# Optimization experiments

Hardware: AMD Instinct MI355X
Metric: run time of the kernel (lower is better)

The kernel has to match this reference:

```python
import jax, jax.numpy as jnp
import numpy as np

N_USERS = 100000
N_ITEMS = 50000
D = 64
IMG_D = 1024
TXT_D = 384
N_EDGES = 2000000
GNN_LAYERS = 2
CAT_RATE = 0.55
NORM_SCALE = 1.0


def setup_inputs() -> dict:
    key = jax.random.key(0)
    ks = jax.random.split(key, 12)
    return {
        "image_feats": jax.random.normal(ks[0], (N_ITEMS, IMG_D), jnp.float32),
        "text_feats": jax.random.normal(ks[1], (N_ITEMS, TXT_D), jnp.float32),
        "user_emb": jax.random.normal(ks[2], (N_USERS, D), jnp.float32) * 0.1,
        "item_emb": jax.random.normal(ks[3], (N_ITEMS, D), jnp.float32) * 0.1,
        "W_img": jax.random.normal(ks[4], (IMG_D, D), jnp.float32) / np.sqrt(IMG_D),
        "b_img": jnp.zeros((D,), jnp.float32),
        "W_txt": jax.random.normal(ks[5], (TXT_D, D), jnp.float32) / np.sqrt(TXT_D),
        "b_txt": jnp.zeros((D,), jnp.float32),
        "val_ui": jax.random.uniform(ks[6], (N_EDGES,), jnp.float32) * 0.05,
        "val_iu": jax.random.uniform(ks[7], (N_EDGES,), jnp.float32) * 0.05,
        "edge_u": jax.random.randint(ks[8], (N_EDGES,), 0, N_USERS, jnp.int32),
        "edge_i": jax.random.randint(ks[9], (N_EDGES,), 0, N_ITEMS, jnp.int32),
    }


def _l2norm(x, eps=1e-12):
    # F.normalize(x, p=2, dim=1)
    n = jnp.maximum(jnp.linalg.norm(x, axis=1, keepdims=True), eps)
    return x / n


def reference(image_feats, text_feats, user_emb, item_emb,
              W_img, b_img, W_txt, b_txt, val_ui, val_iu, edge_u, edge_i):
    def spmm_ui(X):  # ui_graph @ X : [n_items, d] -> [n_users, d]
        return jax.ops.segment_sum(val_ui[:, None] * X[edge_i], edge_u,
                                   num_segments=N_USERS)

    def spmm_iu(X):  # iu_graph @ X : [n_users, d] -> [n_items, d]
        return jax.ops.segment_sum(val_iu[:, None] * X[edge_u], edge_i,
                                   num_segments=N_ITEMS)

    # prompt_module is None -> prompt_user/prompt_item are zeros, so the
    # feat_prompt terms (normalize of zeros) vanish. Dropout in eval = identity.
    image_feat = image_feats @ W_img + b_img  # [n_items, D]
    text_feat = text_feats @ W_txt + b_txt    # [n_items, D]

    # The original loop recomputes identical values every iteration (image_feat
    # is never updated), so one pass gives the same result.
    image_user = spmm_ui(image_feat)
    image_item = spmm_iu(image_user)
    text_user = spmm_ui(text_feat)
    text_item = spmm_iu(text_user)

    # soft_token_rate * normalize(zeros) == 0 -> id embeddings unchanged
    combined = jnp.concatenate([user_emb, item_emb], axis=0)
    # NormLayer mode 'PN' (PairNorm): center, then scale by mean row norm
    c = combined - combined.mean(axis=0, keepdims=True)
    rownorm_mean = jnp.sqrt(jnp.mean(jnp.sum(c * c, axis=1)) + 1e-6)
    normed = NORM_SCALE * c / rownorm_mean
    u_g, i_g = normed[:N_USERS], normed[N_USERS:]

    u_acc, i_acc = u_g, i_g
    for _ in range(GNN_LAYERS):  # is_softmax=False branch
        u_g = spmm_ui(i_g)
        i_g = spmm_iu(u_g)
        u_acc = u_acc + u_g
        i_acc = i_acc + i_g
    user_embeddings = u_acc / (GNN_LAYERS + 1)
    item_embeddings = i_acc / (GNN_LAYERS + 1)

    u_out = (user_embeddings + CAT_RATE * _l2norm(image_user)
             + CAT_RATE * _l2norm(text_user))
    i_out = (item_embeddings + CAT_RATE * _l2norm(image_item)
             + CAT_RATE * _l2norm(text_item))
    return (u_out, i_out, image_item, text_item, image_user, text_user)
```

## Files before the change

kernel.cpp:

```cpp
#include <hip/hip_runtime.h>
#include <cstdint>
#include <cstddef>

#define N_USERS 100000
#define N_ITEMS 50000
#define DIM     64
#define IMG_D   1024
#define TXT_D   384
#define N_EDGES 2000000
#define N_COMB  (N_USERS + N_ITEMS)

#define OFF_UOUT 0
#define OFF_IOUT (N_USERS * DIM)
#define OFF_IIT  (OFF_IOUT + N_ITEMS * DIM)
#define OFF_TIT  (OFF_IIT + N_ITEMS * DIM)
#define OFF_IUS  (OFF_TIT + N_ITEMS * DIM)
#define OFF_TUS  (OFF_IUS + N_USERS * DIM)

typedef __attribute__((ext_vector_type(8))) short short8;
typedef __attribute__((ext_vector_type(4))) float float4v;
typedef __attribute__((ext_vector_type(4))) unsigned int uint4v;

__device__ __forceinline__ float wave_sum64(float v) {
#pragma unroll
  for (int off = 32; off; off >>= 1) v += __shfl_xor(v, off, 64);
  return v;
}

__device__ __forceinline__ unsigned int pack_bf16(float x, float y) {
  const unsigned int xu = __float_as_uint(x) + 0x8000u;
  const unsigned int yu = __float_as_uint(y) + 0x8000u;
  return (xu >> 16) | (yu & 0xffff0000u);
}

__device__ __forceinline__ float4v fma4(float w, const float4v x, float4v a) {
#pragma unroll
  for (int j = 0; j < 4; ++j) a[j] = fmaf(w, x[j], a[j]);
  return a;
}

__global__ __launch_bounds__(256) void hist_kernel(const int* __restrict__ eu,
                                                   const int* __restrict__ ei,
                                                   int* __restrict__ cu, int* __restrict__ ci,
                                                   int* __restrict__ pe_u, int* __restrict__ pe_i) {
  const int i = blockIdx.x * 256 + threadIdx.x;
  if (i < N_EDGES) {
    pe_u[i] = atomicAdd(&cu[eu[i]], 1);
    pe_i[i] = atomicAdd(&ci[ei[i]], 1);
  }
}

__global__ __launch_bounds__(1024) void scan2_kernel(const int* __restrict__ cnt_u,
                                                     int* __restrict__ rs_u,
                                                     const int* __restrict__ cnt_i,
                                                     int* __restrict__ rs_i) {
  const int* counts;
  int *rs, n;
  if (blockIdx.x == 0) { counts = cnt_u; rs = rs_u; n = N_USERS; }
  else                 { counts = cnt_i; rs = rs_i; n = N_ITEMS; }
  __shared__ int part[1024];
  const int t = threadIdx.x;
  const int chunk = (n + 1023) >> 10;
  const int b = t * chunk;
  const int e = min(b + chunk, n);
  int s = 0;
  for (int j = b; j < e; ++j) s += counts[j];
  part[t] = s;
  __syncthreads();
  for (int off = 1; off < 1024; off <<= 1) {
    const int add = (t >= off) ? part[t - off] : 0;
    __syncthreads();
    part[t] += add;
    __syncthreads();
  }
  int run = (t == 0) ? 0 : part[t - 1];
  for (int j = b; j < e; ++j) {
    rs[j] = run;
    run += counts[j];
  }
  if (t == 1023) rs[n] = part[1023];
}

__global__ __launch_bounds__(256) void fill_kernel(
    const int* __restrict__ eu, const int* __restrict__ ei,
    const float* __restrict__ vui, const float* __restrict__ viu,
    const int* __restrict__ pe_u, const int* __restrict__ pe_i,
    const int* __restrict__ rs_u, const int* __restrict__ rs_i,
    int* __restrict__ col_u, float* __restrict__ w_u,
    int* __restrict__ col_i, float* __restrict__ w_i) {
  const int i = blockIdx.x * 256 + threadIdx.x;
  if (i < N_EDGES) {
    const int u = eu[i], it = ei[i];
    const int p = rs_u[u] + pe_u[i];
    const int q = rs_i[it] + pe_i[i];
    col_u[p] = it;
    w_u[p] = vui[i];
    col_i[q] = u;
    w_i[q] = viu[i];
  }
}

__global__ __launch_bounds__(256) void wswizzle_kernel(const float* __restrict__ Wimg,
                                                       const float* __restrict__ Wtxt,
                                                       unsigned short* __restrict__ WBimg,
                                                       unsigned short* __restrict__ WBtxt) {
  int t = blockIdx.x * 256 + threadIdx.x;
  const float* W;
  unsigned short* WB;
  if (t < 8192) { W = Wimg; WB = WBimg; }
  else if (t < 8192 + 3072) { t -= 8192; W = Wtxt; WB = WBtxt; }
  else return;
  const int frag = t >> 6;
  const int lane = t & 63;
  const int K0idx = frag >> 2;
  const int n0idx = frag & 3;
  const int k0 = K0idx * 32 + ((lane >> 4) << 3);
  const int c = n0idx * 16 + (lane & 15);
  unsigned short us[8];
#pragma unroll
  for (int j = 0; j < 8; ++j) {
    const unsigned int b = __float_as_uint(W[(size_t)(k0 + j) * 64 + c]) + 0x8000u;
    us[j] = (unsigned short)(b >> 16);
  }
  uint4v o;
  o.x = (unsigned int)us[0] | ((unsigned int)us[1] << 16);
  o.y = (unsigned int)us[2] | ((unsigned int)us[3] << 16);
  o.z = (unsigned int)us[4] | ((unsigned int)us[5] << 16);
  o.w = (unsigned int)us[6] | ((unsigned int)us[7] << 16);
  *reinterpret_cast<uint4v*>(WB + (size_t)t * 8) = o;
}

__global__ __launch_bounds__(256) void mfma_gemm_kernel(
    const float* __restrict__ Ximg, const unsigned short* __restrict__ WBimg,
    const float* __restrict__ bimg,
    const float* __restrict__ Xtxt, const unsigned short* __restrict__ WBtxt,
    const float* __restrict__ btxt,
    float* __restrict__ feat128) {
  const int TILES_IMG = N_ITEMS / 16;
  const int wv = threadIdx.x >> 6;
  const int lane = threadIdx.x & 63;
  int tile = blockIdx.x * 4 + wv;
  if (tile >= 2 * TILES_IMG) return;

  const float* X;
  const unsigned short* WB;
  const float* bias;
  int K, nK0, c0;
  if (tile < TILES_IMG) { X = Ximg; WB = WBimg; bias = bimg; K = IMG_D; nK0 = IMG_D / 32; c0 = 0; }
  else { tile -= TILES_IMG; X = Xtxt; WB = WBtxt; bias = btxt; K = TXT_D; nK0 = TXT_D / 32; c0 = 64; }

  const int row0 = tile * 16;
  const int m = lane & 15;
  const int koff = (lane >> 4) << 3;
  const float* __restrict__ xp = X + (size_t)(row0 + m) * K + koff;
  const short8* __restrict__ wb8 = reinterpret_cast<const short8*>(WB);

  float4v acc[4];
#pragma unroll
  for (int n0 = 0; n0 < 4; ++n0) acc[n0] = (float4v){0.f, 0.f, 0.f, 0.f};

  for (int K0 = 0; K0 < nK0; ++K0) {
    const float4 xa = *reinterpret_cast<const float4*>(xp + K0 * 32);
    const float4 xb = *reinterpret_cast<const float4*>(xp + K0 * 32 + 4);
    uint4v au;
    au.x = pack_bf16(xa.x, xa.y);
    au.y = pack_bf16(xa.z, xa.w);
    au.z = pack_bf16(xb.x, xb.y);
    au.w = pack_bf16(xb.z, xb.w);
    const short8 af = __builtin_bit_cast(short8, au);
#pragma unroll
    for (int n0 = 0; n0 < 4; ++n0) {
      const short8 bf = wb8[(size_t)(K0 * 4 + n0) * 64 + lane];
      acc[n0] = __builtin_amdgcn_mfma_f32_16x16x32_bf16(af, bf, acc[n0], 0, 0, 0);
    }
  }

  const int crow = (lane >> 4) << 2;
  const int ccol = lane & 15;
#pragma unroll
  for (int n0 = 0; n0 < 4; ++n0) {
    const float bv = bias[n0 * 16 + ccol];
#pragma unroll
    for (int r = 0; r < 4; ++r) {
      feat128[(size_t)(row0 + crow + r) * 128 + c0 + n0 * 16 + ccol] = acc[n0][r] + bv;
    }
  }
}

__global__ __launch_bounds__(256) void stats_kernel(const float* __restrict__ ue,
                                                    const float* __restrict__ ie,
                                                    float* __restrict__ stats) {
  const int t = threadIdx.x;
  const int lane = t & 63;
  float cs = 0.f, ss = 0.f;
  const size_t total = (size_t)N_COMB * DIM;
  const size_t ubound = (size_t)N_USERS * DIM;
  const size_t stride = (size_t)gridDim.x * blockDim.x;
  for (size_t i = (size_t)blockIdx.x * blockDim.x + t; i < total; i += stride) {
    const float v = (i < ubound) ? ue[i] : ie[i - ubound];
    cs += v;
    ss += v * v;
  }
  ss = wave_sum64(ss);
  __shared__ float lcol[4][64];
  __shared__ float lss[4];
  const int wv = t >> 6;
  lcol[wv][lane] = cs;
  if (lane == 0) lss[wv] = ss;
  __syncthreads();
  if (wv == 0) {
    const float c = lcol[0][lane] + lcol[1][lane] + lcol[2][lane] + lcol[3][lane];
    atomicAdd(&stats[lane], c);
    if (lane == 0) atomicAdd(&stats[64], lss[0] + lss[1] + lss[2] + lss[3]);
  }
}

__global__ void finalize_kernel(float* __restrict__ stats) {
  const int d = threadIdx.x;
  const float ssum = stats[64];
  const float m = stats[d] / (float)N_COMB;
  const float m2sum = wave_sum64(m * m);
  const float tot = ssum - (float)N_COMB * m2sum;
  const float rnm = sqrtf(tot / (float)N_COMB + 1e-6f);
  stats[d] = m;
  if (d == 0) stats[64] = 1.f / rnm;
}

__global__ __launch_bounds__(256) void normalize_kernel(
    const float* __restrict__ ue, const float* __restrict__ ie, const float* __restrict__ stats,
    float* __restrict__ uacc, float* __restrict__ iacc, float* __restrict__ i0) {
  const int lane = threadIdx.x & 63;
  const float m = stats[lane];
  const float inv = stats[64];
  const size_t total = (size_t)N_COMB * DIM;
  const size_t ubound = (size_t)N_USERS * DIM;
  const size_t stride = (size_t)gridDim.x * blockDim.x;
  for (size_t i = (size_t)blockIdx.x * blockDim.x + threadIdx.x; i < total; i += stride) {
    if (i < ubound) {
      uacc[i] = (ue[i] - m) * inv;
    } else {
      const size_t j = i - ubound;
      const float v = (ie[j] - m) * inv;
      iacc[j] = v;
      i0[j] = v;
    }
  }
}

__global__ __launch_bounds__(256) void spmm_triple_kernel(
    const int* __restrict__ rs, const int* __restrict__ col, const float* __restrict__ w,
    const float* __restrict__ X1, int s1, const float* __restrict__ X2, int s2,
    const float* __restrict__ X3, int s3,
    float* __restrict__ O1, float* __restrict__ O2, float* __restrict__ O3,
    float* __restrict__ acc, int nrows) {
  const int lane = threadIdx.x & 63;
  const int wv = __builtin_amdgcn_readfirstlane(threadIdx.x >> 6);
  const int r = blockIdx.x * 4 + wv;
  if (r >= nrows) return;
  const int q = lane >> 4;
  const int l = lane & 15;
  const int s = rs[r], e = rs[r + 1];
  float4v a1 = {0.f, 0.f, 0.f, 0.f};
  float4v a2 = {0.f, 0.f, 0.f, 0.f};
  float4v a3 = {0.f, 0.f, 0.f, 0.f};
  int k = s + q;
  for (; k + 4 < e; k += 8) {
    const int c0 = col[k];
    const int c1 = col[k + 4];
    const float w0 = w[k];
    const float w1 = w[k + 4];
    const float4v x10 = *reinterpret_cast<const float4v*>(X1 + (size_t)c0 * s1 + l * 4);
    const float4v x20 = *reinterpret_cast<const float4v*>(X2 + (size_t)c0 * s2 + l * 4);
    const float4v x30 = *reinterpret_cast<const float4v*>(X3 + (size_t)c0 * s3 + l * 4);
    const float4v x11 = *reinterpret_cast<const float4v*>(X1 + (size_t)c1 * s1 + l * 4);
    const float4v x21 = *reinterpret_cast<const float4v*>(X2 + (size_t)c1 * s2 + l * 4);
    const float4v x31 = *reinterpret_cast<const float4v*>(X3 + (size_t)c1 * s3 + l * 4);
    a1 = fma4(w0, x10, a1);
    a2 = fma4(w0, x20, a2);
    a3 = fma4(w0, x30, a3);
    a1 = fma4(w1, x11, a1);
    a2 = fma4(w1, x21, a2);
    a3 = fma4(w1, x31, a3);
  }
  if (k < e) {
    const float w0 = w[k];
    const int c0 = col[k];
    a1 = fma4(w0, *reinterpret_cast<const float4v*>(X1 + (size_t)c0 * s1 + l * 4), a1);
    a2 = fma4(w0, *reinterpret_cast<const float4v*>(X2 + (size_t)c0 * s2 + l * 4), a2);
    a3 = fma4(w0, *reinterpret_cast<const float4v*>(X3 + (size_t)c0 * s3 + l * 4), a3);
  }
#pragma unroll
  for (int j = 0; j < 4; ++j) {
    a1[j] += __shfl_xor(a1[j], 16, 64);
    a1[j] += __shfl_xor(a1[j], 32, 64);
    a2[j] += __shfl_xor(a2[j], 16, 64);
    a2[j] += __shfl_xor(a2[j], 32, 64);
    a3[j] += __shfl_xor(a3[j], 16, 64);
    a3[j] += __shfl_xor(a3[j], 32, 64);
  }
  if (q == 0) {
    const size_t o = (size_t)r * 64 + l * 4;
    *reinterpret_cast<float4v*>(O1 + o) = a1;
    *reinterpret_cast<float4v*>(O2 + o) = a2;
    *reinterpret_cast<float4v*>(O3 + o) = a3;
    float4v av = *reinterpret_cast<const float4v*>(acc + o);
#pragma unroll
    for (int j = 0; j < 4; ++j) av[j] += a3[j];
    *reinterpret_cast<float4v*>(acc + o) = av;
  }
}

__global__ __launch_bounds__(256) void spmm_final_kernel(
    const int* __restrict__ rs, const int* __restrict__ col, const float* __restrict__ w,
    const float* __restrict__ X, float* __restrict__ O,
    const float* __restrict__ P, const float* __restrict__ Q,
    float* __restrict__ accio, int nrows) {
  const int lane = threadIdx.x & 63;
  const int wv = __builtin_amdgcn_readfirstlane(threadIdx.x >> 6);
  const int r = blockIdx.x * 4 + wv;
  if (r >= nrows) return;
  const int q = lane >> 4;
  const int l = lane & 15;
  const int s = rs[r], e = rs[r + 1];
  float4v a = {0.f, 0.f, 0.f, 0.f};
  int k = s + q;
  for (; k + 4 < e; k += 8) {
    const int c0 = col[k];
    const int c1 = col[k + 4];
    const float w0 = w[k];
    const float w1 = w[k + 4];
    const float4v x0 = *reinterpret_cast<const float4v*>(X + (size_t)c0 * 64 + l * 4);
    const float4v x1 = *reinterpret_cast<const float4v*>(X + (size_t)c1 * 64 + l * 4);
    a = fma4(w0, x0, a);
    a = fma4(w1, x1, a);
  }
  if (k < e) {
    a = fma4(w[k], *reinterpret_cast<const float4v*>(X + (size_t)col[k] * 64 + l * 4), a);
  }
#pragma unroll
  for (int j = 0; j < 4; ++j) {
    a[j] += __shfl_xor(a[j], 16, 64);
    a[j] += __shfl_xor(a[j], 32, 64);
  }
  const size_t o = (size_t)r * 64 + l * 4;
  const float4v p = *reinterpret_cast<const float4v*>(P + o);
  const float4v qv = *reinterpret_cast<const float4v*>(Q + o);
  float ps = p[0] * p[0] + p[1] * p[1] + p[2] * p[2] + p[3] * p[3];
  float qs = qv[0] * qv[0] + qv[1] * qv[1] + qv[2] * qv[2] + qv[3] * qv[3];
#pragma unroll
  for (int off = 8; off; off >>= 1) {
    ps += __shfl_xor(ps, off, 64);
    qs += __shfl_xor(qs, off, 64);
  }
  const float pn = 0.55f / fmaxf(sqrtf(ps), 1e-12f);
  const float qn = 0.55f / fmaxf(sqrtf(qs), 1e-12f);
  if (q == 0) {
    if (O) *reinterpret_cast<float4v*>(O + o) = a;
    float4v av = *reinterpret_cast<const float4v*>(accio + o);
#pragma unroll
    for (int j = 0; j < 4; ++j) {
      av[j] = (av[j] + a[j]) * (1.0f / 3.0f) + pn * p[j] + qn * qv[j];
    }
    *reinterpret_cast<float4v*>(accio + o) = av;
  }
}

extern "C" void kernel_launch(void* const* d_in, const int* in_sizes, int n_in,
                              void* d_out, int out_size, void* d_ws, size_t ws_size,
                              hipStream_t stream) {
  const float* image_feats = (const float*)d_in[0];
  const float* text_feats = (const float*)d_in[1];
  const float* user_emb = (const float*)d_in[2];
  const float* item_emb = (const float*)d_in[3];
  const float* W_img = (const float*)d_in[4];
  const float* b_img = (const float*)d_in[5];
  const float* W_txt = (const float*)d_in[6];
  const float* b_txt = (const float*)d_in[7];
  const float* val_ui = (const float*)d_in[8];
  const float* val_iu = (const float*)d_in[9];
  const int* edge_u = (const int*)d_in[10];
  const int* edge_i = (const int*)d_in[11];

  float* out = (float*)d_out;
  float* u_acc = out + OFF_UOUT;
  float* i_acc = out + OFF_IOUT;
  float* img_item = out + OFF_IIT;
  float* txt_item = out + OFF_TIT;
  float* img_user = out + OFF_IUS;
  float* txt_user = out + OFF_TUS;

  char* wsb = (char*)d_ws;
  size_t off = 0;
  auto take = [&](size_t bytes) -> void* {
    void* p = wsb + off;
    off += (bytes + 255) & ~(size_t)255;
    return p;
  };
  float* feat128 = (float*)take((size_t)N_ITEMS * 128 * 4);
  float* i0 = (float*)take((size_t)N_ITEMS * DIM * 4);
  float* i1 = (float*)take((size_t)N_ITEMS * DIM * 4);
  float* u1 = (float*)take((size_t)N_USERS * DIM * 4);
  int* col_u = (int*)take((size_t)N_EDGES * 4);
  float* w_u = (float*)take((size_t)N_EDGES * 4);
  int* col_i = (int*)take((size_t)N_EDGES * 4);
  float* w_i = (float*)take((size_t)N_EDGES * 4);
  int* rs_u = (int*)take((N_USERS + 1) * 4);
  int* rs_i = (int*)take((N_ITEMS + 1) * 4);
  int* cnt_u = (int*)take((size_t)N_USERS * 4);
  int* cnt_i = (int*)take((size_t)N_ITEMS * 4);
  unsigned short* WBimg = (unsigned short*)take((size_t)8192 * 8 * 2);
  unsigned short* WBtxt = (unsigned short*)take((size_t)3072 * 8 * 2);
  float* stats = (float*)take(65 * 4);

  int* pe_u = (int*)feat128;
  int* pe_i = pe_u + N_EDGES;

  hipMemsetAsync(cnt_u, 0, (size_t)N_USERS * 4, stream);
  hipMemsetAsync(cnt_i, 0, (size_t)N_ITEMS * 4, stream);
  hipMemsetAsync(stats, 0, 65 * 4, stream);

  const int eblk = (N_EDGES + 255) / 256;
  hist_kernel<<<eblk, 256, 0, stream>>>(edge_u, edge_i, cnt_u, cnt_i, pe_u, pe_i);
  scan2_kernel<<<2, 1024, 0, stream>>>(cnt_u, rs_u, cnt_i, rs_i);
  fill_kernel<<<eblk, 256, 0, stream>>>(edge_u, edge_i, val_ui, val_iu, pe_u, pe_i,
                                        rs_u, rs_i, col_u, w_u, col_i, w_i);

  wswizzle_kernel<<<44, 256, 0, stream>>>(W_img, W_txt, WBimg, WBtxt);
  const int ntiles = 2 * (N_ITEMS / 16);
  mfma_gemm_kernel<<<(ntiles + 3) / 4, 256, 0, stream>>>(image_feats, WBimg, b_img,
                                                         text_feats, WBtxt, b_txt, feat128);

  stats_kernel<<<2048, 256, 0, stream>>>(user_emb, item_emb, stats);
  finalize_kernel<<<1, 64, 0, stream>>>(stats);
  normalize_kernel<<<2048, 256, 0, stream>>>(user_emb, item_emb, stats, u_acc, i_acc, i0);

  spmm_triple_kernel<<<N_USERS / 4, 256, 0, stream>>>(
      rs_u, col_u, w_u, feat128, 128, feat128 + 64, 128, i0, 64,
      img_user, txt_user, u1, u_acc, N_USERS);
  spmm_triple_kernel<<<N_ITEMS / 4, 256, 0, stream>>>(
      rs_i, col_i, w_i, img_user, 64, txt_user, 64, u1, 64,
      img_item, txt_item, i1, i_acc, N_ITEMS);
  spmm_final_kernel<<<N_USERS / 4, 256, 0, stream>>>(
      rs_u, col_u, w_u, i1, u1, img_user, txt_user, u_acc, N_USERS);
  spmm_final_kernel<<<N_ITEMS / 4, 256, 0, stream>>>(
      rs_i, col_i, w_i, u1, nullptr, img_item, txt_item, i_acc, N_ITEMS);
}
```

Before: 1.547 ms.

## Store SpMM gather operands as interleaved fp16 rows to halve gather traffic

The GEMM outputs, the normalized item embeddings and the intermediate propagation results are now stored as fp16 instead of fp32. Operands that are gathered together are interleaved into one 192-wide row per node (image, text and ID features), so each edge gathers from a single contiguous row. Accumulation stays in fp32, and the final outputs stay fp32. This targets the memory bandwidth of the random row gathers in the SpMM kernels. In exchange it adds fp16 rounding to intermediate values, which could affect accuracy tolerance.

```diff
diff --git a/kernel.cpp b/kernel.cpp
--- a/kernel.cpp
+++ b/kernel.cpp
@@ -20,6 +20,7 @@
 typedef __attribute__((ext_vector_type(8))) short short8;
 typedef __attribute__((ext_vector_type(4))) float float4v;
 typedef __attribute__((ext_vector_type(4))) unsigned int uint4v;
+typedef __attribute__((ext_vector_type(4))) _Float16 half4v;
 
 __device__ __forceinline__ float wave_sum64(float v) {
 #pragma unroll
@@ -33,10 +34,17 @@
   return (xu >> 16) | (yu & 0xffff0000u);
 }
 
-__device__ __forceinline__ float4v fma4(float w, const float4v x, float4v a) {
-#pragma unroll
-  for (int j = 0; j < 4; ++j) a[j] = fmaf(w, x[j], a[j]);
+__device__ __forceinline__ float4v fma4h(float w, const half4v x, float4v a) {
+#pragma unroll
+  for (int j = 0; j < 4; ++j) a[j] = fmaf(w, (float)x[j], a[j]);
   return a;
+}
+
+__device__ __forceinline__ half4v to_h4(const float4v a) {
+  half4v h;
+#pragma unroll
+  for (int j = 0; j < 4; ++j) h[j] = (_Float16)a[j];
+  return h;
 }
 
 __global__ __launch_bounds__(256) void hist_kernel(const int* __restrict__ eu,
@@ -135,7 +143,7 @@
     const float* __restrict__ bimg,
     const float* __restrict__ Xtxt, const unsigned short* __restrict__ WBtxt,
     const float* __restrict__ btxt,
-    float* __restrict__ feat128) {
+    _Float16* __restrict__ g_items) {
   const int TILES_IMG = N_ITEMS / 16;
   const int wv = threadIdx.x >> 6;
   const int lane = threadIdx.x & 63;
@@ -182,7 +190,8 @@
     const float bv = bias[n0 * 16 + ccol];
 #pragma unroll
     for (int r = 0; r < 4; ++r) {
-      feat128[(size_t)(row0 + crow + r) * 128 + c0 + n0 * 16 + ccol] = acc[n0][r] + bv;
+      g_items[(size_t)(row0 + crow + r) * 192 + c0 + n0 * 16 + ccol] =
+          (_Float16)(acc[n0][r] + bv);
     }
   }
 }
@@ -228,7 +237,7 @@
 
 __global__ __launch_bounds__(256) void normalize_kernel(
     const float* __restrict__ ue, const float* __restrict__ ie, const float* __restrict__ stats,
-    float* __restrict__ uacc, float* __restrict__ iacc, float* __restrict__ i0) {
+    float* __restrict__ uacc, float* __restrict__ iacc, _Float16* __restrict__ g_items) {
   const int lane = threadIdx.x & 63;
   const float m = stats[lane];
   const float inv = stats[64];
@@ -242,17 +251,17 @@
       const size_t j = i - ubound;
       const float v = (ie[j] - m) * inv;
       iacc[j] = v;
-      i0[j] = v;
+      g_items[(j >> 6) * 192 + 128 + (j & 63)] = (_Float16)v;
     }
   }
 }
 
 __global__ __launch_bounds__(256) void spmm_triple_kernel(
     const int* __restrict__ rs, const int* __restrict__ col, const float* __restrict__ w,
-    const float* __restrict__ X1, int s1, const float* __restrict__ X2, int s2,
-    const float* __restrict__ X3, int s3,
-    float* __restrict__ O1, float* __restrict__ O2, float* __restrict__ O3,
-    float* __restrict__ acc, int nrows) {
+    const _Float16* __restrict__ G,
+    float* __restrict__ O1, float* __restrict__ O2,
+    float* __restrict__ acc,
+    _Float16* __restrict__ gout192, _Float16* __restrict__ gout64, int nrows) {
   const int lane = threadIdx.x & 63;
   const int wv = __builtin_amdgcn_readfirstlane(threadIdx.x >> 6);
   const int r = blockIdx.x * 4 + wv;
@@ -269,25 +278,27 @@
     const int c1 = col[k + 4];
     const float w0 = w[k];
     const float w1 = w[k + 4];
-    const float4v x10 = *reinterpret_cast<const float4v*>(X1 + (size_t)c0 * s1 + l * 4);
-    const float4v x20 = *reinterpret_cast<const float4v*>(X2 + (size_t)c0 * s2 + l * 4);
-    const float4v x30 = *reinterpret_cast<const float4v*>(X3 + (size_t)c0 * s3 + l * 4);
-    const float4v x11 = *reinterpret_cast<const float4v*>(X1 + (size_t)c1 * s1 + l * 4);
-    const float4v x21 = *reinterpret_cast<const float4v*>(X2 + (size_t)c1 * s2 + l * 4);
-    const float4v x31 = *reinterpret_cast<const float4v*>(X3 + (size_t)c1 * s3 + l * 4);
-    a1 = fma4(w0, x10, a1);
-    a2 = fma4(w0, x20, a2);
-    a3 = fma4(w0, x30, a3);
-    a1 = fma4(w1, x11, a1);
-    a2 = fma4(w1, x21, a2);
-    a3 = fma4(w1, x31, a3);
+    const _Float16* g0 = G + (size_t)c0 * 192 + l * 4;
+    const _Float16* g1 = G + (size_t)c1 * 192 + l * 4;
+    const half4v x10 = *reinterpret_cast<const half4v*>(g0);
+    const half4v x20 = *reinterpret_cast<const half4v*>(g0 + 64);
+    const half4v x30 = *reinterpret_cast<const half4v*>(g0 + 128);
+    const half4v x11 = *reinterpret_cast<const half4v*>(g1);
+    const half4v x21 = *reinterpret_cast<const half4v*>(g1 + 64);
+    const half4v x31 = *reinterpret_cast<const half4v*>(g1 + 128);
+    a1 = fma4h(w0, x10, a1);
+    a2 = fma4h(w0, x20, a2);
+    a3 = fma4h(w0, x30, a3);
+    a1 = fma4h(w1, x11, a1);
+    a2 = fma4h(w1, x21, a2);
+    a3 = fma4h(w1, x31, a3);
   }
   if (k < e) {
     const float w0 = w[k];
-    const int c0 = col[k];
-    a1 = fma4(w0, *reinterpret_cast<const float4v*>(X1 + (size_t)c0 * s1 + l * 4), a1);
-    a2 = fma4(w0, *reinterpret_cast<const float4v*>(X2 + (size_t)c0 * s2 + l * 4), a2);
-    a3 = fma4(w0, *reinterpret_cast<const float4v*>(X3 + (size_t)c0 * s3 + l * 4), a3);
+    const _Float16* g0 = G + (size_t)col[k] * 192 + l * 4;
+    a1 = fma4h(w0, *reinterpret_cast<const half4v*>(g0), a1);
+    a2 = fma4h(w0, *reinterpret_cast<const half4v*>(g0 + 64), a2);
+    a3 = fma4h(w0, *reinterpret_cast<const half4v*>(g0 + 128), a3);
   }
 #pragma unroll
   for (int j = 0; j < 4; ++j) {
@@ -302,17 +313,24 @@
     const size_t o = (size_t)r * 64 + l * 4;
     *reinterpret_cast<float4v*>(O1 + o) = a1;
     *reinterpret_cast<float4v*>(O2 + o) = a2;
-    *reinterpret_cast<float4v*>(O3 + o) = a3;
     float4v av = *reinterpret_cast<const float4v*>(acc + o);
 #pragma unroll
     for (int j = 0; j < 4; ++j) av[j] += a3[j];
     *reinterpret_cast<float4v*>(acc + o) = av;
+    if (gout192) {
+      _Float16* gr = gout192 + (size_t)r * 192 + l * 4;
+      *reinterpret_cast<half4v*>(gr) = to_h4(a1);
+      *reinterpret_cast<half4v*>(gr + 64) = to_h4(a2);
+      *reinterpret_cast<half4v*>(gr + 128) = to_h4(a3);
+    } else {
+      *reinterpret_cast<half4v*>(gout64 + o) = to_h4(a3);
+    }
   }
 }
 
 __global__ __launch_bounds__(256) void spmm_final_kernel(
     const int* __restrict__ rs, const int* __restrict__ col, const float* __restrict__ w,
-    const float* __restrict__ X, float* __restrict__ O,
+    const _Float16* __restrict__ X, _Float16* __restrict__ GO,
     const float* __restrict__ P, const float* __restrict__ Q,
     float* __restrict__ accio, int nrows) {
   const int lane = threadIdx.x & 63;
@@ -329,13 +347,13 @@
     const int c1 = col[k + 4];
     const float w0 = w[k];
     const float w1 = w[k + 4];
-    const float4v x0 = *reinterpret_cast<const float4v*>(X + (size_t)c0 * 64 + l * 4);
-    const float4v x1 = *reinterpret_cast<const float4v*>(X + (size_t)c1 * 64 + l * 4);
-    a = fma4(w0, x0, a);
-    a = fma4(w1, x1, a);
+    const half4v x0 = *reinterpret_cast<const half4v*>(X + (size_t)c0 * 64 + l * 4);
+    const half4v x1 = *reinterpret_cast<const half4v*>(X + (size_t)c1 * 64 + l * 4);
+    a = fma4h(w0, x0, a);
+    a = fma4h(w1, x1, a);
   }
   if (k < e) {
-    a = fma4(w[k], *reinterpret_cast<const float4v*>(X + (size_t)col[k] * 64 + l * 4), a);
+    a = fma4h(w[k], *reinterpret_cast<const half4v*>(X + (size_t)col[k] * 64 + l * 4), a);
   }
 #pragma unroll
   for (int j = 0; j < 4; ++j) {
@@ -355,7 +373,7 @@
   const float pn = 0.55f / fmaxf(sqrtf(ps), 1e-12f);
   const float qn = 0.55f / fmaxf(sqrtf(qs), 1e-12f);
   if (q == 0) {
-    if (O) *reinterpret_cast<float4v*>(O + o) = a;
+    if (GO) *reinterpret_cast<half4v*>(GO + o) = to_h4(a);
     float4v av = *reinterpret_cast<const float4v*>(accio + o);
 #pragma unroll
     for (int j = 0; j < 4; ++j) {
@@ -396,10 +414,10 @@
     off += (bytes + 255) & ~(size_t)255;
     return p;
   };
-  float* feat128 = (float*)take((size_t)N_ITEMS * 128 * 4);
-  float* i0 = (float*)take((size_t)N_ITEMS * DIM * 4);
-  float* i1 = (float*)take((size_t)N_ITEMS * DIM * 4);
-  float* u1 = (float*)take((size_t)N_USERS * DIM * 4);
+  _Float16* g_items = (_Float16*)take((size_t)N_ITEMS * 192 * 2);
+  _Float16* g_users = (_Float16*)take((size_t)N_USERS * 192 * 2);
+  _Float16* g_i1 = (_Float16*)take((size_t)N_ITEMS * 64 * 2);
+  _Float16* g_u2 = (_Float16*)take((size_t)N_USERS * 64 * 2);
   int* col_u = (int*)take((size_t)N_EDGES * 4);
   float* w_u = (float*)take((size_t)N_EDGES * 4);
   int* col_i = (int*)take((size_t)N_EDGES * 4);
@@ -412,7 +430,7 @@
   unsigned short* WBtxt = (unsigned short*)take((size_t)3072 * 8 * 2);
   float* stats = (float*)take(65 * 4);
 
-  int* pe_u = (int*)feat128;
+  int* pe_u = (int*)g_users;
   int* pe_i = pe_u + N_EDGES;
 
   hipMemsetAsync(cnt_u, 0, (size_t)N_USERS * 4, stream);
@@ -428,20 +446,18 @@
   wswizzle_kernel<<<44, 256, 0, stream>>>(W_img, W_txt, WBimg, WBtxt);
   const int ntiles = 2 * (N_ITEMS / 16);
   mfma_gemm_kernel<<<(ntiles + 3) / 4, 256, 0, stream>>>(image_feats, WBimg, b_img,
-                                                         text_feats, WBtxt, b_txt, feat128);
+                                                         text_feats, WBtxt, b_txt, g_items);
 
   stats_kernel<<<2048, 256, 0, stream>>>(user_emb, item_emb, stats);
   finalize_kernel<<<1, 64, 0, stream>>>(stats);
-  normalize_kernel<<<2048, 256, 0, stream>>>(user_emb, item_emb, stats, u_acc, i_acc, i0);
+  normalize_kernel<<<2048, 256, 0, stream>>>(user_emb, item_emb, stats, u_acc, i_acc, g_items);
 
   spmm_triple_kernel<<<N_USERS / 4, 256, 0, stream>>>(
-      rs_u, col_u, w_u, feat128, 128, feat128 + 64, 128, i0, 64,
-      img_user, txt_user, u1, u_acc, N_USERS);
+      rs_u, col_u, w_u, g_items, img_user, txt_user, u_acc, g_users, nullptr, N_USERS);
   spmm_triple_kernel<<<N_ITEMS / 4, 256, 0, stream>>>(
-      rs_i, col_i, w_i, img_user, 64, txt_user, 64, u1, 64,
-      img_item, txt_item, i1, i_acc, N_ITEMS);
+      rs_i, col_i, w_i, g_users, img_item, txt_item, i_acc, nullptr, g_i1, N_ITEMS);
   spmm_final_kernel<<<N_USERS / 4, 256, 0, stream>>>(
-      rs_u, col_u, w_u, i1, u1, img_user, txt_user, u_acc, N_USERS);
+      rs_u, col_u, w_u, g_i1, g_u2, img_user, txt_user, u_acc, N_USERS);
   spmm_final_kernel<<<N_ITEMS / 4, 256, 0, stream>>>(
-      rs_i, col_i, w_i, u1, nullptr, img_item, txt_item, i_acc, N_ITEMS);
-}
+      rs_i, col_i, w_i, g_u2, nullptr, img_item, txt_item, i_acc, N_ITEMS);
+}
```

Result: faster. 1.310 ms (-15.3%).
